# Kernel tuning notes

Measured on AMD Instinct MI355X. Metric: run time of the kernel, lower is better.

The kernel has to match this reference:

```python
import jax, jax.numpy as jnp
import numpy as np

B, D, L = 4, 256, 4096

def setup_inputs() -> dict:
    key = jax.random.key(0)
    k1, k2, k3 = jax.random.split(key, 3)
    query = jax.random.normal(k1, (B, D, L), dtype=jnp.float32)
    context = jax.random.normal(k2, (B, D, L), dtype=jnp.float32)
    W_in = jax.random.normal(k3, (D, D), dtype=jnp.float32) * 0.02
    b_in = jnp.zeros((D,), dtype=jnp.float32)
    return {"query": query, "context": context, "W_in": W_in, "b_in": b_in}

def reference(query, context, W_in, b_in):
    # inputs are [B, D, L]; module transposes to [B, L, D]
    q = jnp.transpose(query, (0, 2, 1))    # [B, O, D]
    c = jnp.transpose(context, (0, 2, 1))  # [B, Q, D]
    # 'general': linear_in applied to query only (torch Linear: x @ W^T + b)
    q = q @ W_in.T + b_in
    # unscaled Luong attention: QK^T -> softmax -> A V
    scores = jnp.einsum('bod,bqd->boq', q, c)          # [B, O, Q]
    weights = jax.nn.softmax(scores, axis=-1)          # [B, O, Q]
    out = jnp.einsum('boq,bqd->bod', weights, c)       # [B, O, D]
    return (out, weights)
```

## Files before the change

### kernel.cpp

```cpp
#include <hip/hip_runtime.h>


#define BATCH 4
#define DDIM  256
#define LSEQ  4096
#define TQ    64

typedef float    f32x4 __attribute__((ext_vector_type(4)));
typedef _Float16 f16x8 __attribute__((ext_vector_type(8)));
typedef _Float16 f16x4 __attribute__((ext_vector_type(4)));

__device__ __forceinline__ void gld16(const void* g, void* l) {
  __builtin_amdgcn_global_load_lds((const __attribute__((address_space(1))) void*)g,
                                   (__attribute__((address_space(3))) void*)l, 16, 0, 0);
}

__global__ __launch_bounds__(256) void transpose_cast(
    const float* __restrict__ q_in, const float* __restrict__ c_in,
    _Float16* __restrict__ q_out, _Float16* __restrict__ c_out)
{
  __shared__ float tile[64][68];
  const int which = blockIdx.z >> 2;
  const int b     = blockIdx.z & 3;
  const float* __restrict__ src = which ? c_in : q_in;
  _Float16* __restrict__ dst    = which ? c_out : q_out;
  const int l0 = blockIdx.x * 64, d0 = blockIdx.y * 64;
  const int tid = threadIdx.x;
  const int tr = tid >> 4, tc = (tid & 15) << 2;
#pragma unroll
  for (int i = 0; i < 4; ++i) {
    int d = tr + i * 16;
    f32x4 v = *(const f32x4*)(src + ((size_t)b * DDIM + d0 + d) * LSEQ + l0 + tc);
    *(f32x4*)&tile[d][tc] = v;
  }
  __syncthreads();
#pragma unroll
  for (int i = 0; i < 4; ++i) {
    int l = tr + i * 16;
    f16x4 h;
    h[0] = (_Float16)tile[tc + 0][l];
    h[1] = (_Float16)tile[tc + 1][l];
    h[2] = (_Float16)tile[tc + 2][l];
    h[3] = (_Float16)tile[tc + 3][l];
    *(f16x4*)(dst + ((size_t)b * LSEQ + l0 + l) * DDIM + d0 + tc) = h;
  }
}

__global__ __launch_bounds__(256) void wconv(const float* __restrict__ w,
                                             _Float16* __restrict__ w16) {
  int i = (blockIdx.x * 256 + threadIdx.x) * 4;
  f32x4 v = *(const f32x4*)(w + i);
  f16x4 h;
  h[0] = (_Float16)v[0]; h[1] = (_Float16)v[1];
  h[2] = (_Float16)v[2]; h[3] = (_Float16)v[3];
  *(f16x4*)(w16 + i) = h;
}

__global__ __launch_bounds__(256) void castD(const float* __restrict__ c_in,
                                             _Float16* __restrict__ cD16) {
  size_t i = ((size_t)blockIdx.x * 256 + threadIdx.x) * 8;
  f32x4 a = *(const f32x4*)(c_in + i);
  f32x4 b = *(const f32x4*)(c_in + i + 4);
  f16x8 h;
  h[0] = (_Float16)a[0]; h[1] = (_Float16)a[1];
  h[2] = (_Float16)a[2]; h[3] = (_Float16)a[3];
  h[4] = (_Float16)b[0]; h[5] = (_Float16)b[1];
  h[6] = (_Float16)b[2]; h[7] = (_Float16)b[3];
  *(f16x8*)(cD16 + i) = h;
}

__global__ __launch_bounds__(256) void linear_q(
    const _Float16* __restrict__ qT16, const _Float16* __restrict__ W16,
    const float* __restrict__ bias, _Float16* __restrict__ qw16)
{
  const int tid = threadIdx.x;
  const int wv = tid >> 6, ln = tid & 63, g = ln >> 4, c16 = ln & 15;
  const size_t r0 = (size_t)blockIdx.x * 64 + wv * 16;

  f16x8 qa[8];
  const _Float16* qrow = qT16 + (r0 + c16) * DDIM + g * 8;
#pragma unroll
  for (int kk = 0; kk < 8; ++kk) qa[kk] = *(const f16x8*)(qrow + kk * 32);

  f32x4 acc[16];
#pragma unroll
  for (int n = 0; n < 16; ++n) acc[n] = f32x4{0.f, 0.f, 0.f, 0.f};

#pragma unroll 2
  for (int kk = 0; kk < 8; ++kk) {
#pragma unroll
    for (int n = 0; n < 16; ++n) {
      f16x8 bf = *(const f16x8*)(W16 + (n * 16 + c16) * DDIM + kk * 32 + g * 8);
      acc[n] = __builtin_amdgcn_mfma_f32_16x16x32_f16(qa[kk], bf, acc[n], 0, 0, 0);
    }
  }
#pragma unroll
  for (int n = 0; n < 16; ++n) {
    float bb = bias[n * 16 + c16];
#pragma unroll
    for (int r = 0; r < 4; ++r)
      qw16[(r0 + 4 * g + r) * DDIM + n * 16 + c16] = (_Float16)(acc[n][r] + bb);
  }
}

__global__ __launch_bounds__(512, 2) void attn_main(
    const _Float16* __restrict__ qw16,
    const _Float16* __restrict__ cT16,
    const _Float16* __restrict__ cD16,
    float* __restrict__ outp,
    float* __restrict__ wgt)
{
  __shared__ __align__(16) char smem[2][32768];
  __shared__ __align__(16) char wbuf[8192];
  __shared__ __align__(16) char obuf[65536];
  __shared__ float redbuf[4][64];

  const int tid = threadIdx.x;
  const int wv  = tid >> 6;
  const int qw  = wv & 3;
  const int oh  = wv >> 2;
  const int ln  = tid & 63;
  const int g   = ln >> 4;
  const int c16 = ln & 15;

  const int lin   = blockIdx.y * 64 + blockIdx.x;
  const int b     = (lin & 7) >> 1;
  const int otile = ((lin >> 3) << 1) | (lin & 1);
  const int o0    = otile * 64;
  const int bo    = b * LSEQ + o0;

  const _Float16* __restrict__ cbase = cT16 + (size_t)b * LSEQ * DDIM;
  const _Float16* __restrict__ cDb   = cD16 + (size_t)b * DDIM * LSEQ;

  f16x8 qb[2][8];
#pragma unroll
  for (int of = 0; of < 2; ++of)
#pragma unroll
    for (int kk = 0; kk < 8; ++kk)
      qb[of][kk] = *(const f16x8*)(qw16 +
          ((size_t)(bo + oh * 32 + of * 16 + c16) << 8) + kk * 32 + g * 8);

  float lsum0 = 0.f, lsum1 = 0.f;

  auto loadA = [&](int t, f16x8 aa[8]) {
    const _Float16* src = cbase + ((size_t)(t * TQ + qw * 16 + c16) << 8) + g * 8;
#pragma unroll
    for (int kk = 0; kk < 8; ++kk) aa[kk] = *(const f16x8*)(src + kk * 32);
  };
  auto ascore = [&](const f16x8 aa[8]) {
    f32x4 s0{0.f, 0.f, 0.f, 0.f}, s1{0.f, 0.f, 0.f, 0.f};
#pragma unroll
    for (int kk = 0; kk < 8; ++kk) {
      s0 = __builtin_amdgcn_mfma_f32_16x16x32_f16(aa[kk], qb[0][kk], s0, 0, 0, 0);
      s1 = __builtin_amdgcn_mfma_f32_16x16x32_f16(aa[kk], qb[1][kk], s1, 0, 0, 0);
    }
#pragma unroll
    for (int r = 0; r < 4; ++r) {
      lsum0 += __expf(s0[r]);
      lsum1 += __expf(s1[r]);
    }
  };

  {
    f16x8 aaA[8], aaB[8];
    loadA(0, aaA);
    for (int t = 0; t < LSEQ / TQ; t += 2) {
      loadA(t + 1, aaB);
      ascore(aaA);
      if (t + 2 < LSEQ / TQ) loadA(t + 2, aaA);
      ascore(aaB);
    }
  }

  lsum0 += __shfl_xor(lsum0, 16); lsum0 += __shfl_xor(lsum0, 32);
  lsum1 += __shfl_xor(lsum1, 16); lsum1 += __shfl_xor(lsum1, 32);
  if (ln < 16) {
    redbuf[qw][oh * 32 + ln]      = lsum0;
    redbuf[qw][oh * 32 + 16 + ln] = lsum1;
  }
  __syncthreads();
  float invl[2];
#pragma unroll
  for (int of = 0; of < 2; ++of) {
    int o = oh * 32 + of * 16 + c16;
    invl[of] = 1.0f / (redbuf[0][o] + redbuf[1][o] + redbuf[2][o] + redbuf[3][o]);
  }

  auto issue_dma = [&](int t, int pp) {
#pragma unroll
    for (int i = 0; i < 4; ++i) {
      unsigned x  = (unsigned)tid * 16 + i * 8192;
      unsigned q  = x >> 9;
      unsigned db = (x & 511u) ^ ((q & 7u) << 4);
      gld16(cbase + ((size_t)(t * TQ + q) << 8) + (db >> 1), &smem[pp][x]);
    }
  };

  f32x4 oacc[4][4];
#pragma unroll
  for (int m = 0; m < 4; ++m)
#pragma unroll
    for (int nf = 0; nf < 4; ++nf) oacc[m][nf] = f32x4{0.f, 0.f, 0.f, 0.f};

  int p = 0;
  issue_dma(0, 0);
  for (int t = 0; t < LSEQ / TQ; ++t) {
    const int q0 = t * TQ;
    if (t == 0) asm volatile("s_waitcnt vmcnt(0)" ::: "memory");
    else        asm volatile("s_waitcnt vmcnt(2)" ::: "memory");
    __builtin_amdgcn_s_barrier();
    __builtin_amdgcn_sched_barrier(0);

    f16x8 bv[4];
#pragma unroll
    for (int nf = 0; nf < 4; ++nf)
      bv[nf] = *(const f16x8*)(cDb +
          ((size_t)(qw * 64 + nf * 16 + c16) << 12) + q0 + oh * 32 + g * 8);

    if (t < LSEQ / TQ - 1) issue_dma(t + 1, p ^ 1);

    const char* cl = smem[p];
    f32x4 sa0{0.f, 0.f, 0.f, 0.f}, sa1{0.f, 0.f, 0.f, 0.f};
#pragma unroll
    for (int kk = 0; kk < 8; ++kk) {
      unsigned off = (unsigned)((qw * 16 + c16) * 512 + kk * 64 + g * 16) ^
                     ((unsigned)(c16 & 7) << 4);
      f16x8 af = *(const f16x8*)(cl + off);
      sa0 = __builtin_amdgcn_mfma_f32_16x16x32_f16(af, qb[0][kk], sa0, 0, 0, 0);
      sa1 = __builtin_amdgcn_mfma_f32_16x16x32_f16(af, qb[1][kk], sa1, 0, 0, 0);
    }

#pragma unroll
    for (int of = 0; of < 2; ++of) {
      f32x4 sv = of ? sa1 : sa0;
      f32x4 wv4;
      f16x4 wh;
#pragma unroll
      for (int r = 0; r < 4; ++r) {
        float w = __expf(sv[r]) * invl[of];
        wv4[r] = w;
        wh[r]  = (_Float16)w;
      }
      int o = oh * 32 + of * 16 + c16;
      *(f32x4*)(wgt + ((size_t)(bo + o) << 12) + q0 + qw * 16 + 4 * g) = wv4;
      unsigned wb = (unsigned)(o * 128 + qw * 32 + g * 8) ^ ((unsigned)(o & 7) << 4);
      *(f16x4*)(wbuf + wb) = wh;
    }
    asm volatile("s_waitcnt lgkmcnt(0)" ::: "memory");
    __builtin_amdgcn_s_barrier();
    __builtin_amdgcn_sched_barrier(0);

#pragma unroll
    for (int m = 0; m < 4; ++m) {
      unsigned off = (unsigned)((m * 16 + c16) * 128 + oh * 64 + g * 16) ^
                     ((unsigned)(c16 & 7) << 4);
      f16x8 wa = *(const f16x8*)(wbuf + off);
#pragma unroll
      for (int nf = 0; nf < 4; ++nf)
        oacc[m][nf] =
            __builtin_amdgcn_mfma_f32_16x16x32_f16(wa, bv[nf], oacc[m][nf], 0, 0, 0);
    }
    p ^= 1;
  }

  if (oh == 1) {
#pragma unroll
    for (int m = 0; m < 4; ++m)
#pragma unroll
      for (int nf = 0; nf < 4; ++nf)
        *(f32x4*)(obuf + qw * 16384 + (m * 4 + nf) * 1024 + ln * 16) = oacc[m][nf];
  }
  __syncthreads();
  if (oh == 0) {
#pragma unroll
    for (int m = 0; m < 4; ++m)
#pragma unroll
      for (int nf = 0; nf < 4; ++nf) {
        f32x4 o2 = *(const f32x4*)(obuf + qw * 16384 + (m * 4 + nf) * 1024 + ln * 16);
        f32x4 o  = oacc[m][nf] + o2;
#pragma unroll
        for (int r = 0; r < 4; ++r)
          outp[((size_t)(bo + m * 16 + 4 * g + r) << 8) + qw * 64 + nf * 16 + c16] = o[r];
      }
  }
}

extern "C" void kernel_launch(void* const* d_in, const int* in_sizes, int n_in,
                              void* d_out, int out_size, void* d_ws, size_t ws_size,
                              hipStream_t stream) {
  const float* query   = (const float*)d_in[0];
  const float* context = (const float*)d_in[1];
  const float* W_in    = (const float*)d_in[2];
  const float* b_in    = (const float*)d_in[3];

  float* outp = (float*)d_out;
  float* wgt  = outp + (size_t)BATCH * LSEQ * DDIM;

  const size_t NELEM = (size_t)BATCH * LSEQ * DDIM;
  _Float16* qT16 = (_Float16*)d_ws;
  _Float16* cT16 = qT16 + NELEM;
  _Float16* qw16 = cT16 + NELEM;
  _Float16* W16  = qw16 + NELEM;
  _Float16* cD16 = qT16;

  transpose_cast<<<dim3(LSEQ / 64, DDIM / 64, 2 * BATCH), 256, 0, stream>>>(
      query, context, qT16, cT16);
  wconv<<<(DDIM * DDIM) / 1024, 256, 0, stream>>>(W_in, W16);
  linear_q<<<(BATCH * LSEQ) / 64, 256, 0, stream>>>(qT16, W16, b_in, qw16);
  castD<<<(int)(NELEM / 2048), 256, 0, stream>>>(context, cD16);
  attn_main<<<dim3(64, BATCH), 512, 0, stream>>>(qw16, cT16, cD16, outp, wgt);
}
```

Before: 324.6 us.

## Split attention into separate row-sum and split-K PV kernels with atomic accumulation

Moves the softmax denominator pass out of the main attention kernel into its own kernel (1024 blocks, each covering half of the key sequence), with partial sums written to workspace. The PV kernel now splits the key dimension in two, doubling the grid to 512 blocks, and accumulates output with atomicAdd after a memset. It also reuses the staging shared memory for the output reduction buffer so more blocks fit per CU. The aim is better occupancy and CU fill on the 256-CU device, at the cost of an extra launch, a memset, atomic traffic on the output, and recomputed scores in both kernels.

```diff
diff --git a/kernel.cpp b/kernel.cpp
--- a/kernel.cpp
+++ b/kernel.cpp
@@ -103,17 +103,77 @@
   }
 }
 
-__global__ __launch_bounds__(512, 2) void attn_main(
+__global__ __launch_bounds__(256, 4) void attn_lsum(
+    const _Float16* __restrict__ qw16,
+    const _Float16* __restrict__ cT16,
+    float* __restrict__ lsum_ws)
+{
+  __shared__ float red[4][32];
+  const int tid = threadIdx.x;
+  const int qw  = tid >> 6;
+  const int ln  = tid & 63;
+  const int g   = ln >> 4;
+  const int c16 = ln & 15;
+
+  const int lin = blockIdx.x;
+  const int b   = (lin & 7) >> 1;
+  const int r2  = ((lin >> 3) << 1) | (lin & 1);
+  const int otA = r2 >> 1;
+  const int qh  = r2 & 1;
+  const int o0  = otA * 32;
+
+  const _Float16* __restrict__ cbase = cT16 + (size_t)b * LSEQ * DDIM;
+
+  f16x8 qb[2][8];
+#pragma unroll
+  for (int of = 0; of < 2; ++of)
+#pragma unroll
+    for (int kk = 0; kk < 8; ++kk)
+      qb[of][kk] = *(const f16x8*)(qw16 +
+          ((size_t)(b * LSEQ + o0 + of * 16 + c16) << 8) + kk * 32 + g * 8);
+
+  float lsum0 = 0.f, lsum1 = 0.f;
+  for (int t = 0; t < 32; ++t) {
+    const int tq = qh * 32 + t;
+    f16x8 aa[8];
+    const _Float16* src = cbase + ((size_t)(tq * TQ + qw * 16 + c16) << 8) + g * 8;
+#pragma unroll
+    for (int kk = 0; kk < 8; ++kk) aa[kk] = *(const f16x8*)(src + kk * 32);
+    f32x4 s0{0.f, 0.f, 0.f, 0.f}, s1{0.f, 0.f, 0.f, 0.f};
+#pragma unroll
+    for (int kk = 0; kk < 8; ++kk) {
+      s0 = __builtin_amdgcn_mfma_f32_16x16x32_f16(aa[kk], qb[0][kk], s0, 0, 0, 0);
+      s1 = __builtin_amdgcn_mfma_f32_16x16x32_f16(aa[kk], qb[1][kk], s1, 0, 0, 0);
+    }
+#pragma unroll
+    for (int r = 0; r < 4; ++r) {
+      lsum0 += __expf(s0[r]);
+      lsum1 += __expf(s1[r]);
+    }
+  }
+  lsum0 += __shfl_xor(lsum0, 16); lsum0 += __shfl_xor(lsum0, 32);
+  lsum1 += __shfl_xor(lsum1, 16); lsum1 += __shfl_xor(lsum1, 32);
+  if (ln < 16) {
+    red[qw][ln]      = lsum0;
+    red[qw][16 + ln] = lsum1;
+  }
+  __syncthreads();
+  if (tid < 32)
+    lsum_ws[((size_t)(b * 2 + qh)) * LSEQ + o0 + tid] =
+        red[0][tid] + red[1][tid] + red[2][tid] + red[3][tid];
+}
+
+__global__ __launch_bounds__(512, 4) void attn_pv(
     const _Float16* __restrict__ qw16,
     const _Float16* __restrict__ cT16,
     const _Float16* __restrict__ cD16,
+    const float* __restrict__ lsum_ws,
     float* __restrict__ outp,
     float* __restrict__ wgt)
 {
   __shared__ __align__(16) char smem[2][32768];
   __shared__ __align__(16) char wbuf[8192];
-  __shared__ __align__(16) char obuf[65536];
-  __shared__ float redbuf[4][64];
+  char* obuf = &smem[0][0];
 
   const int tid = threadIdx.x;
   const int wv  = tid >> 6;
@@ -123,14 +183,25 @@
   const int g   = ln >> 4;
   const int c16 = ln & 15;
 
-  const int lin   = blockIdx.y * 64 + blockIdx.x;
-  const int b     = (lin & 7) >> 1;
-  const int otile = ((lin >> 3) << 1) | (lin & 1);
-  const int o0    = otile * 64;
-  const int bo    = b * LSEQ + o0;
+  const int lin = blockIdx.x;
+  const int b   = (lin & 7) >> 1;
+  const int r2  = ((lin >> 3) << 1) | (lin & 1);
+  const int ot  = r2 >> 1;
+  const int qh  = r2 & 1;
+  const int o0  = ot * 64;
+  const int bo  = b * LSEQ + o0;
+  const int qbase = qh * (LSEQ / 2);
 
   const _Float16* __restrict__ cbase = cT16 + (size_t)b * LSEQ * DDIM;
   const _Float16* __restrict__ cDb   = cD16 + (size_t)b * DDIM * LSEQ;
+
+  float invl[2];
+#pragma unroll
+  for (int of = 0; of < 2; ++of) {
+    int o = o0 + oh * 32 + of * 16 + c16;
+    invl[of] = 1.0f / (lsum_ws[(size_t)(b * 2) * LSEQ + o] +
+                       lsum_ws[(size_t)(b * 2 + 1) * LSEQ + o]);
+  }
 
   f16x8 qb[2][8];
 #pragma unroll
@@ -139,52 +210,6 @@
     for (int kk = 0; kk < 8; ++kk)
       qb[of][kk] = *(const f16x8*)(qw16 +
           ((size_t)(bo + oh * 32 + of * 16 + c16) << 8) + kk * 32 + g * 8);
-
-  float lsum0 = 0.f, lsum1 = 0.f;
-
-  auto loadA = [&](int t, f16x8 aa[8]) {
-    const _Float16* src = cbase + ((size_t)(t * TQ + qw * 16 + c16) << 8) + g * 8;
-#pragma unroll
-    for (int kk = 0; kk < 8; ++kk) aa[kk] = *(const f16x8*)(src + kk * 32);
-  };
-  auto ascore = [&](const f16x8 aa[8]) {
-    f32x4 s0{0.f, 0.f, 0.f, 0.f}, s1{0.f, 0.f, 0.f, 0.f};
-#pragma unroll
-    for (int kk = 0; kk < 8; ++kk) {
-      s0 = __builtin_amdgcn_mfma_f32_16x16x32_f16(aa[kk], qb[0][kk], s0, 0, 0, 0);
-      s1 = __builtin_amdgcn_mfma_f32_16x16x32_f16(aa[kk], qb[1][kk], s1, 0, 0, 0);
-    }
-#pragma unroll
-    for (int r = 0; r < 4; ++r) {
-      lsum0 += __expf(s0[r]);
-      lsum1 += __expf(s1[r]);
-    }
-  };
-
-  {
-    f16x8 aaA[8], aaB[8];
-    loadA(0, aaA);
-    for (int t = 0; t < LSEQ / TQ; t += 2) {
-      loadA(t + 1, aaB);
-      ascore(aaA);
-      if (t + 2 < LSEQ / TQ) loadA(t + 2, aaA);
-      ascore(aaB);
-    }
-  }
-
-  lsum0 += __shfl_xor(lsum0, 16); lsum0 += __shfl_xor(lsum0, 32);
-  lsum1 += __shfl_xor(lsum1, 16); lsum1 += __shfl_xor(lsum1, 32);
-  if (ln < 16) {
-    redbuf[qw][oh * 32 + ln]      = lsum0;
-    redbuf[qw][oh * 32 + 16 + ln] = lsum1;
-  }
-  __syncthreads();
-  float invl[2];
-#pragma unroll
-  for (int of = 0; of < 2; ++of) {
-    int o = oh * 32 + of * 16 + c16;
-    invl[of] = 1.0f / (redbuf[0][o] + redbuf[1][o] + redbuf[2][o] + redbuf[3][o]);
-  }
 
   auto issue_dma = [&](int t, int pp) {
 #pragma unroll
@@ -192,7 +217,7 @@
       unsigned x  = (unsigned)tid * 16 + i * 8192;
       unsigned q  = x >> 9;
       unsigned db = (x & 511u) ^ ((q & 7u) << 4);
-      gld16(cbase + ((size_t)(t * TQ + q) << 8) + (db >> 1), &smem[pp][x]);
+      gld16(cbase + ((size_t)(qbase + t * TQ + q) << 8) + (db >> 1), &smem[pp][x]);
     }
   };
 
@@ -204,8 +229,8 @@
 
   int p = 0;
   issue_dma(0, 0);
-  for (int t = 0; t < LSEQ / TQ; ++t) {
-    const int q0 = t * TQ;
+  for (int t = 0; t < 32; ++t) {
+    const int q0 = qbase + t * TQ;
     if (t == 0) asm volatile("s_waitcnt vmcnt(0)" ::: "memory");
     else        asm volatile("s_waitcnt vmcnt(2)" ::: "memory");
     __builtin_amdgcn_s_barrier();
@@ -217,7 +242,7 @@
       bv[nf] = *(const f16x8*)(cDb +
           ((size_t)(qw * 64 + nf * 16 + c16) << 12) + q0 + oh * 32 + g * 8);
 
-    if (t < LSEQ / TQ - 1) issue_dma(t + 1, p ^ 1);
+    if (t < 31) issue_dma(t + 1, p ^ 1);
 
     const char* cl = smem[p];
     f32x4 sa0{0.f, 0.f, 0.f, 0.f}, sa1{0.f, 0.f, 0.f, 0.f};
@@ -263,6 +288,7 @@
     p ^= 1;
   }
 
+  __syncthreads();
   if (oh == 1) {
 #pragma unroll
     for (int m = 0; m < 4; ++m)
@@ -280,7 +306,8 @@
         f32x4 o  = oacc[m][nf] + o2;
 #pragma unroll
         for (int r = 0; r < 4; ++r)
-          outp[((size_t)(bo + m * 16 + 4 * g + r) << 8) + qw * 64 + nf * 16 + c16] = o[r];
+          atomicAdd(&outp[((size_t)(bo + m * 16 + 4 * g + r) << 8) +
+                          qw * 64 + nf * 16 + c16], o[r]);
       }
   }
 }
@@ -301,6 +328,7 @@
   _Float16* cT16 = qT16 + NELEM;
   _Float16* qw16 = cT16 + NELEM;
   _Float16* W16  = qw16 + NELEM;
+  float*    lsum_ws = (float*)(W16 + 65536);
   _Float16* cD16 = qT16;
 
   transpose_cast<<<dim3(LSEQ / 64, DDIM / 64, 2 * BATCH), 256, 0, stream>>>(
@@ -308,5 +336,7 @@
   wconv<<<(DDIM * DDIM) / 1024, 256, 0, stream>>>(W_in, W16);
   linear_q<<<(BATCH * LSEQ) / 64, 256, 0, stream>>>(qT16, W16, b_in, qw16);
   castD<<<(int)(NELEM / 2048), 256, 0, stream>>>(context, cD16);
-  attn_main<<<dim3(64, BATCH), 512, 0, stream>>>(qw16, cT16, cD16, outp, wgt);
-}
+  hipMemsetAsync(outp, 0, NELEM * sizeof(float), stream);
+  attn_lsum<<<1024, 256, 0, stream>>>(qw16, cT16, lsum_ws);
+  attn_pv<<<512, 512, 0, stream>>>(qw16, cT16, cD16, lsum_ws, outp, wgt);
+}
```

Result: slower. 591.3 us (+82.2%).

## Stage context tiles via LDS DMA in softmax-denominator pass and alias output buffer

Applied to the files above, without the earlier changes.

The first pass that computes softmax denominators now loads context tiles into double-buffered LDS with global_load_lds DMA instead of per-wave register loads. This halves redundant global reads, since the two o-halves shared the same context rows. The pass prefetches tile 0 again at the end, so the second pass starts with data already resident. The 64KB output reduction buffer is aliased onto the staging buffers and the occupancy hint in launch bounds is dropped. This lowers the LDS footprint but adds barriers and a full vmcnt(0) wait every iteration of the first pass.

```diff
diff --git a/kernel.cpp b/kernel.cpp
--- a/kernel.cpp
+++ b/kernel.cpp
@@ -103,7 +103,7 @@
   }
 }
 
-__global__ __launch_bounds__(512, 2) void attn_main(
+__global__ __launch_bounds__(512) void attn_main(
     const _Float16* __restrict__ qw16,
     const _Float16* __restrict__ cT16,
     const _Float16* __restrict__ cD16,
@@ -112,8 +112,8 @@
 {
   __shared__ __align__(16) char smem[2][32768];
   __shared__ __align__(16) char wbuf[8192];
-  __shared__ __align__(16) char obuf[65536];
   __shared__ float redbuf[4][64];
+  char* obuf = &smem[0][0];
 
   const int tid = threadIdx.x;
   const int wv  = tid >> 6;
@@ -140,36 +140,41 @@
       qb[of][kk] = *(const f16x8*)(qw16 +
           ((size_t)(bo + oh * 32 + of * 16 + c16) << 8) + kk * 32 + g * 8);
 
+  auto issue_dma = [&](int t, int pp) {
+#pragma unroll
+    for (int i = 0; i < 4; ++i) {
+      unsigned x  = (unsigned)tid * 16 + i * 8192;
+      unsigned q  = x >> 9;
+      unsigned db = (x & 511u) ^ ((q & 7u) << 4);
+      gld16(cbase + ((size_t)(t * TQ + q) << 8) + (db >> 1), &smem[pp][x]);
+    }
+  };
+
   float lsum0 = 0.f, lsum1 = 0.f;
-
-  auto loadA = [&](int t, f16x8 aa[8]) {
-    const _Float16* src = cbase + ((size_t)(t * TQ + qw * 16 + c16) << 8) + g * 8;
-#pragma unroll
-    for (int kk = 0; kk < 8; ++kk) aa[kk] = *(const f16x8*)(src + kk * 32);
-  };
-  auto ascore = [&](const f16x8 aa[8]) {
-    f32x4 s0{0.f, 0.f, 0.f, 0.f}, s1{0.f, 0.f, 0.f, 0.f};
+  int p = 0;
+  issue_dma(0, 0);
+  for (int t = 0; t < LSEQ / TQ; ++t) {
+    asm volatile("s_waitcnt vmcnt(0)" ::: "memory");
+    __builtin_amdgcn_s_barrier();
+    issue_dma(t < LSEQ / TQ - 1 ? t + 1 : 0, p ^ 1);
+    __builtin_amdgcn_sched_barrier(0);
+
+    const char* cl = smem[p];
+    f32x4 sa0{0.f, 0.f, 0.f, 0.f}, sa1{0.f, 0.f, 0.f, 0.f};
 #pragma unroll
     for (int kk = 0; kk < 8; ++kk) {
-      s0 = __builtin_amdgcn_mfma_f32_16x16x32_f16(aa[kk], qb[0][kk], s0, 0, 0, 0);
-      s1 = __builtin_amdgcn_mfma_f32_16x16x32_f16(aa[kk], qb[1][kk], s1, 0, 0, 0);
+      unsigned off = (unsigned)((qw * 16 + c16) * 512 + kk * 64 + g * 16) ^
+                     ((unsigned)(c16 & 7) << 4);
+      f16x8 af = *(const f16x8*)(cl + off);
+      sa0 = __builtin_amdgcn_mfma_f32_16x16x32_f16(af, qb[0][kk], sa0, 0, 0, 0);
+      sa1 = __builtin_amdgcn_mfma_f32_16x16x32_f16(af, qb[1][kk], sa1, 0, 0, 0);
     }
 #pragma unroll
     for (int r = 0; r < 4; ++r) {
-      lsum0 += __expf(s0[r]);
-      lsum1 += __expf(s1[r]);
-    }
-  };
-
-  {
-    f16x8 aaA[8], aaB[8];
-    loadA(0, aaA);
-    for (int t = 0; t < LSEQ / TQ; t += 2) {
-      loadA(t + 1, aaB);
-      ascore(aaA);
-      if (t + 2 < LSEQ / TQ) loadA(t + 2, aaA);
-      ascore(aaB);
-    }
+      lsum0 += __expf(sa0[r]);
+      lsum1 += __expf(sa1[r]);
+    }
+    p ^= 1;
   }
 
   lsum0 += __shfl_xor(lsum0, 16); lsum0 += __shfl_xor(lsum0, 32);
@@ -186,24 +191,12 @@
     invl[of] = 1.0f / (redbuf[0][o] + redbuf[1][o] + redbuf[2][o] + redbuf[3][o]);
   }
 
-  auto issue_dma = [&](int t, int pp) {
-#pragma unroll
-    for (int i = 0; i < 4; ++i) {
-      unsigned x  = (unsigned)tid * 16 + i * 8192;
-      unsigned q  = x >> 9;
-      unsigned db = (x & 511u) ^ ((q & 7u) << 4);
-      gld16(cbase + ((size_t)(t * TQ + q) << 8) + (db >> 1), &smem[pp][x]);
-    }
-  };
-
   f32x4 oacc[4][4];
 #pragma unroll
   for (int m = 0; m < 4; ++m)
 #pragma unroll
     for (int nf = 0; nf < 4; ++nf) oacc[m][nf] = f32x4{0.f, 0.f, 0.f, 0.f};
 
-  int p = 0;
-  issue_dma(0, 0);
   for (int t = 0; t < LSEQ / TQ; ++t) {
     const int q0 = t * TQ;
     if (t == 0) asm volatile("s_waitcnt vmcnt(0)" ::: "memory");
@@ -263,6 +256,7 @@
     p ^= 1;
   }
 
+  __syncthreads();
   if (oh == 1) {
 #pragma unroll
     for (int m = 0; m < 4; ++m)
```

Result: faster. 271.2 us (-16.4%).
